# Performance work log

Hardware: AMD Instinct MI355X
Metric: run time of the kernel (lower is better)

The kernel has to match this reference:

```python
import jax, jax.numpy as jnp
import numpy as np

N = 100000
E = 800000
IN_DIM = 256
HEADS = 8
OUT_DIM = 32
OUT_ALL = HEADS * OUT_DIM  # 256 == IN_DIM -> residual is Identity
NEG_SLOPE = 0.2


def setup_inputs() -> dict:
    key = jax.random.key(0)
    ks = jax.random.split(key, 10)
    s_in = 1.0 / np.sqrt(IN_DIM)
    x = jax.random.normal(ks[0], (N, IN_DIM), dtype=jnp.float32)
    edge_index = jax.random.randint(ks[1], (2, E), 0, N, dtype=jnp.int64)
    Wl = jax.random.normal(ks[2], (IN_DIM, OUT_ALL), dtype=jnp.float32) * s_in
    bl = jnp.zeros((OUT_ALL,), dtype=jnp.float32)
    Wr = jax.random.normal(ks[3], (IN_DIM, OUT_ALL), dtype=jnp.float32) * s_in
    br = jnp.zeros((OUT_ALL,), dtype=jnp.float32)
    att = jax.random.normal(ks[4], (HEADS, OUT_DIM), dtype=jnp.float32) * (1.0 / np.sqrt(OUT_DIM))
    bias = jnp.zeros((OUT_ALL,), dtype=jnp.float32)
    gamma = jnp.ones((OUT_ALL,), dtype=jnp.float32)
    beta = jnp.zeros((OUT_ALL,), dtype=jnp.float32)
    return {"x": x, "edge_index": edge_index, "Wl": Wl, "bl": bl, "Wr": Wr,
            "br": br, "att": att, "bias": bias, "gamma": gamma, "beta": beta}


def reference(x, edge_index, Wl, bl, Wr, br, att, bias, gamma, beta):
    src, dst = edge_index[0], edge_index[1]
    # GATv2: separate transforms for source (lin_l) and target (lin_r)
    x_l = (x @ Wl + bl).reshape(N, HEADS, OUT_DIM)  # messages / source side
    x_r = (x @ Wr + br).reshape(N, HEADS, OUT_DIM)  # target side
    # edge-wise GATv2 score: a^T LeakyReLU(x_j + x_i)
    s = jax.nn.leaky_relu(x_l[src] + x_r[dst], NEG_SLOPE)  # [E, H, D]
    e = jnp.einsum('ehd,hd->eh', s, att)                   # [E, H]
    # segment softmax over incoming edges of each destination node
    m = jax.ops.segment_max(e, dst, num_segments=N)        # [N, H]
    p = jnp.exp(e - m[dst])                                # [E, H]
    denom = jax.ops.segment_sum(p, dst, num_segments=N)    # [N, H]
    denom = jnp.where(denom == 0, 1.0, denom)
    alpha = p / denom[dst]                                 # [E, H]
    # scatter-sum aggregate of alpha * lin_l(x_src)
    msg = alpha[:, :, None] * x_l[src]                     # [E, H, D]
    out = jax.ops.segment_sum(msg, dst, num_segments=N)    # [N, H, D]
    y = out.reshape(N, OUT_ALL) + bias
    # residual is Identity since in_dim == heads*out_dim
    z = y + x
    # LayerNorm then ELU
    mu = jnp.mean(z, axis=-1, keepdims=True)
    var = jnp.var(z, axis=-1, keepdims=True)
    zn = (z - mu) * jax.lax.rsqrt(var + 1e-5) * gamma + beta
    return jax.nn.elu(zn)
```

## Files before the change

### kernel.cpp

```cpp
#include <hip/hip_runtime.h>
#include <hip/hip_bf16.h>

#define NN 100000
#define EE 800000
#define DALL 256
#define NEG 0.2f

#define CNT_BLOCKS 3125
#define CVTW_BLOCKS 128
#define CVTX_BLOCKS 2048

typedef __attribute__((ext_vector_type(8))) short bf16x8;
typedef __attribute__((ext_vector_type(4))) float f32x4;

static __device__ __forceinline__ ushort f2b(float f) {
    __hip_bfloat16 h = __float2bfloat16(f);
    return *reinterpret_cast<ushort*>(&h);
}
static __device__ __forceinline__ float b2f(ushort u) {
    union { float f; unsigned v; } c; c.v = ((unsigned)u) << 16; return c.f;
}
static __device__ __forceinline__ void unpack8(uint4 u, float* v) {
    v[0] = b2f((ushort)(u.x & 0xffff)); v[1] = b2f((ushort)(u.x >> 16));
    v[2] = b2f((ushort)(u.y & 0xffff)); v[3] = b2f((ushort)(u.y >> 16));
    v[4] = b2f((ushort)(u.z & 0xffff)); v[5] = b2f((ushort)(u.z >> 16));
    v[6] = b2f((ushort)(u.w & 0xffff)); v[7] = b2f((ushort)(u.w >> 16));
}

__global__ __launch_bounds__(256) void fused_init(
    const float* __restrict__ x, const float* __restrict__ Wl,
    const float* __restrict__ Wr, const int* __restrict__ dst,
    ushort* __restrict__ xb, ushort* __restrict__ Wt, int* __restrict__ cnt)
{
    __shared__ float tile[32][33];
    int b = blockIdx.x;
    if (b < CNT_BLOCKS) {
        int e = b * 256 + threadIdx.x;
        if (e < EE) atomicAdd(&cnt[dst[e]], 1);
        return;
    }
    b -= CNT_BLOCKS;
    if (b < CVTW_BLOCKS) {
        int kt = (b & 7) * 32, nt = (b >> 3) * 32;
        int tx = threadIdx.x & 31, ty = threadIdx.x >> 5;
#pragma unroll
        for (int i = 0; i < 32; i += 8) {
            int k = kt + ty + i, n = nt + tx;
            float v = (n < 256) ? Wl[(size_t)k * 256 + n] : Wr[(size_t)k * 256 + (n - 256)];
            tile[ty + i][tx] = v;
        }
        __syncthreads();
#pragma unroll
        for (int i = 0; i < 32; i += 8) {
            int n = nt + ty + i, k = kt + tx;
            Wt[(size_t)n * 256 + k] = f2b(tile[tx][ty + i]);
        }
        return;
    }
    b -= CVTW_BLOCKS;
    const int total = NN * DALL / 8;
    for (int i = b * 256 + threadIdx.x; i < total; i += CVTX_BLOCKS * 256) {
        float4 a = reinterpret_cast<const float4*>(x)[i * 2];
        float4 c = reinterpret_cast<const float4*>(x)[i * 2 + 1];
        uint4 o;
        o.x = f2b(a.x) | ((unsigned)f2b(a.y) << 16);
        o.y = f2b(a.z) | ((unsigned)f2b(a.w) << 16);
        o.z = f2b(c.x) | ((unsigned)f2b(c.y) << 16);
        o.w = f2b(c.z) | ((unsigned)f2b(c.w) << 16);
        reinterpret_cast<uint4*>(xb)[i] = o;
    }
}

__global__ __launch_bounds__(256) void gemm_dual(
    const ushort* __restrict__ xb,
    const ushort* __restrict__ Wt,
    const float* __restrict__ bl, const float* __restrict__ br,
    ushort* __restrict__ xl, ushort* __restrict__ xr)
{
    __shared__ __align__(16) ushort smem[2][2][128 * 32];

    const int bx = blockIdx.x;
    const int rowBase = (bx >> 2) * 128;
    const int colBase = (bx & 3) * 128;
    const int t = threadIdx.x, lane = t & 63, wave = t >> 6;
    const int wr = (wave >> 1) * 64, wc = (wave & 1) * 64;

    const int sr  = lane >> 2;
    const int sc8 = (lane & 3) * 8;

    f32x4 acc[4][4];
#pragma unroll
    for (int m = 0; m < 4; ++m)
#pragma unroll
        for (int n = 0; n < 4; ++n) acc[m][n] = (f32x4){0.f, 0.f, 0.f, 0.f};

    auto STAGE = [&](int buf, int kb) {
#pragma unroll
        for (int tt = 0; tt < 2; ++tt) {
            int rbase = wave * 32 + tt * 16;
            int r = rbase + sr;
            int ga = rowBase + r; if (ga >= NN) ga = NN - 1;
            const ushort* gpA = xb + (size_t)ga * 256 + kb + sc8;
            ushort* lpA = &smem[buf][0][rbase * 32];
            __builtin_amdgcn_global_load_lds(
                (const __attribute__((address_space(1))) unsigned int*)gpA,
                (__attribute__((address_space(3))) unsigned int*)lpA, 16, 0, 0);
            int gb = colBase + r;
            const ushort* gpB = Wt + (size_t)gb * 256 + kb + sc8;
            ushort* lpB = &smem[buf][1][rbase * 32];
            __builtin_amdgcn_global_load_lds(
                (const __attribute__((address_space(1))) unsigned int*)gpB,
                (__attribute__((address_space(3))) unsigned int*)lpB, 16, 0, 0);
        }
    };

    STAGE(0, 0);
    __syncthreads();

#pragma unroll
    for (int s = 0; s < 8; ++s) {
        if (s < 7) STAGE((s + 1) & 1, (s + 1) * 32);
        const ushort* A = smem[s & 1][0];
        const ushort* B = smem[s & 1][1];
        bf16x8 af[4], bfr[4];
#pragma unroll
        for (int m = 0; m < 4; ++m)
            af[m] = *reinterpret_cast<const bf16x8*>(
                &A[(wr + m * 16 + (lane & 15)) * 32 + (lane >> 4) * 8]);
#pragma unroll
        for (int n = 0; n < 4; ++n)
            bfr[n] = *reinterpret_cast<const bf16x8*>(
                &B[(wc + n * 16 + (lane & 15)) * 32 + (lane >> 4) * 8]);
#pragma unroll
        for (int m = 0; m < 4; ++m)
#pragma unroll
            for (int n = 0; n < 4; ++n)
                acc[m][n] = __builtin_amdgcn_mfma_f32_16x16x32_bf16(
                    af[m], bfr[n], acc[m][n], 0, 0, 0);
        if (s < 7) __syncthreads();
    }

    const bool isL = (colBase < 256);
    ushort* OutP = isL ? xl : xr;
    const float* bvp = isL ? bl : br;
    const int cb0 = colBase & 255;

    int colLoc[4]; float bb[4];
#pragma unroll
    for (int n = 0; n < 4; ++n) {
        colLoc[n] = cb0 + wc + n * 16 + (lane & 15);
        bb[n] = bvp[colLoc[n]];
    }
#pragma unroll
    for (int m = 0; m < 4; ++m) {
        int r0 = rowBase + wr + m * 16 + (lane >> 4) * 4;
#pragma unroll
        for (int r = 0; r < 4; ++r) {
            int row = r0 + r;
            if (row < NN) {
#pragma unroll
                for (int n = 0; n < 4; ++n)
                    OutP[(size_t)row * 256 + colLoc[n]] = f2b(acc[m][n][r] + bb[n]);
            }
        }
    }
}

__global__ __launch_bounds__(256) void scan_part1(const int* __restrict__ cnt,
                                                  int* __restrict__ bsums)
{
    __shared__ int red[256];
    int base = blockIdx.x * 1024 + threadIdx.x * 4;
    int s = 0;
#pragma unroll
    for (int k = 0; k < 4; ++k) { int i = base + k; if (i < NN) s += cnt[i]; }
    red[threadIdx.x] = s; __syncthreads();
    for (int off = 128; off > 0; off >>= 1) {
        if (threadIdx.x < off) red[threadIdx.x] += red[threadIdx.x + off];
        __syncthreads();
    }
    if (threadIdx.x == 0) bsums[blockIdx.x] = red[0];
}

__global__ __launch_bounds__(256) void scan_rowptr(const int* __restrict__ cnt,
                                                   const int* __restrict__ bsums,
                                                   int* __restrict__ rowptr)
{
    __shared__ int redB[256];
    __shared__ int pre[256];
    int tb = threadIdx.x;
    redB[tb] = (tb < (int)blockIdx.x) ? bsums[tb] : 0;
    __syncthreads();
    for (int off = 128; off > 0; off >>= 1) {
        if (tb < off) redB[tb] += redB[tb + off];
        __syncthreads();
    }
    int base0 = redB[0];

    int base = blockIdx.x * 1024 + tb * 4;
    int v[4]; int s = 0;
#pragma unroll
    for (int k = 0; k < 4; ++k) { int i = base + k; v[k] = (i < NN) ? cnt[i] : 0; s += v[k]; }
    pre[tb] = s; __syncthreads();
    for (int off = 1; off < 256; off <<= 1) {
        int tv = (tb >= off) ? pre[tb - off] : 0;
        __syncthreads();
        pre[tb] += tv;
        __syncthreads();
    }
    int excl = pre[tb] - s + base0;
#pragma unroll
    for (int k = 0; k < 4; ++k) {
        int i = base + k;
        if (i < NN) { rowptr[i] = excl; excl += v[k]; }
    }
}

__global__ __launch_bounds__(256) void fill_csr(const int* __restrict__ src,
                                                const int* __restrict__ dst,
                                                int* __restrict__ rowptr,
                                                int* __restrict__ srcs)
{
    int e = blockIdx.x * 256 + threadIdx.x;
    if (e >= EE) return;
    int pos = atomicAdd(&rowptr[dst[e]], 1);
    srcs[pos] = src[e];
}

__global__ __launch_bounds__(256) void aggregate_finalize(
    const ushort* __restrict__ xl, const ushort* __restrict__ xr,
    const int* __restrict__ srcs, const int* __restrict__ rowptr,
    const float* __restrict__ att, const ushort* __restrict__ xb,
    const float* __restrict__ bias, const float* __restrict__ gamma,
    const float* __restrict__ beta, float* __restrict__ out)
{
    int node = blockIdx.x * 4 + (threadIdx.x >> 6);
    if (node >= NN) return;
    int lane = threadIdx.x & 63;
    int half = lane >> 5;
    int dl = lane & 31;
    const int off = dl * 8;

    uint4 xru = *reinterpret_cast<const uint4*>(xr + (size_t)node * DALL + off);
    float xrv[8]; unpack8(xru, xrv);
    float atv[8];
    {
        float4 a0 = *reinterpret_cast<const float4*>(att + off);
        float4 a1 = *reinterpret_cast<const float4*>(att + off + 4);
        atv[0]=a0.x; atv[1]=a0.y; atv[2]=a0.z; atv[3]=a0.w;
        atv[4]=a1.x; atv[5]=a1.y; atv[6]=a1.z; atv[7]=a1.w;
    }

    int beg = node ? rowptr[node - 1] : 0;
    int end = rowptr[node];
    float a[8] = {0.f,0.f,0.f,0.f,0.f,0.f,0.f,0.f};
    float dsum = 0.f;

    for (int base = beg; base < end; base += 8) {
        int j0 = base + half;
        int j1 = base + 2 + half;
        int j2 = base + 4 + half;
        int j3 = base + 6 + half;
        bool k0 = j0 < end, k1 = j1 < end, k2 = j2 < end, k3 = j3 < end;
        int s0 = srcs[k0 ? j0 : beg];
        int s1 = srcs[k1 ? j1 : beg];
        int s2 = srcs[k2 ? j2 : beg];
        int s3 = srcs[k3 ? j3 : beg];
        uint4 g0 = *reinterpret_cast<const uint4*>(xl + (size_t)s0 * DALL + off);
        uint4 g1 = *reinterpret_cast<const uint4*>(xl + (size_t)s1 * DALL + off);
        uint4 g2 = *reinterpret_cast<const uint4*>(xl + (size_t)s2 * DALL + off);
        uint4 g3 = *reinterpret_cast<const uint4*>(xl + (size_t)s3 * DALL + off);
        float v0v[8], v1v[8], v2v[8], v3v[8];
        unpack8(g0, v0v); unpack8(g1, v1v); unpack8(g2, v2v); unpack8(g3, v3v);
        float p0 = 0.f, p1 = 0.f, p2 = 0.f, p3 = 0.f;
#pragma unroll
        for (int i = 0; i < 8; ++i) {
            float z0 = v0v[i] + xrv[i]; p0 += fmaxf(z0, NEG * z0) * atv[i];
            float z1 = v1v[i] + xrv[i]; p1 += fmaxf(z1, NEG * z1) * atv[i];
            float z2 = v2v[i] + xrv[i]; p2 += fmaxf(z2, NEG * z2) * atv[i];
            float z3 = v3v[i] + xrv[i]; p3 += fmaxf(z3, NEG * z3) * atv[i];
        }
        p0 += __shfl_xor(p0, 1); p0 += __shfl_xor(p0, 2);
        p1 += __shfl_xor(p1, 1); p1 += __shfl_xor(p1, 2);
        p2 += __shfl_xor(p2, 1); p2 += __shfl_xor(p2, 2);
        p3 += __shfl_xor(p3, 1); p3 += __shfl_xor(p3, 2);
        float e0 = k0 ? __expf(p0) : 0.f;
        float e1 = k1 ? __expf(p1) : 0.f;
        float e2 = k2 ? __expf(p2) : 0.f;
        float e3 = k3 ? __expf(p3) : 0.f;
#pragma unroll
        for (int i = 0; i < 8; ++i)
            a[i] += e0 * v0v[i] + e1 * v1v[i] + e2 * v2v[i] + e3 * v3v[i];
        dsum += e0 + e1 + e2 + e3;
    }

#pragma unroll
    for (int i = 0; i < 8; ++i) a[i] += __shfl_xor(a[i], 32);
    dsum += __shfl_xor(dsum, 32);
    float inv = dsum > 0.f ? 1.f / dsum : 0.f;

    uint4 xbu = *reinterpret_cast<const uint4*>(xb + (size_t)node * DALL + off);
    float xv[8]; unpack8(xbu, xv);
    float bvv[8], gvv[8], bev[8];
    {
        float4 b0 = *reinterpret_cast<const float4*>(bias + off);
        float4 b1 = *reinterpret_cast<const float4*>(bias + off + 4);
        bvv[0]=b0.x; bvv[1]=b0.y; bvv[2]=b0.z; bvv[3]=b0.w;
        bvv[4]=b1.x; bvv[5]=b1.y; bvv[6]=b1.z; bvv[7]=b1.w;
        float4 g0 = *reinterpret_cast<const float4*>(gamma + off);
        float4 g1 = *reinterpret_cast<const float4*>(gamma + off + 4);
        gvv[0]=g0.x; gvv[1]=g0.y; gvv[2]=g0.z; gvv[3]=g0.w;
        gvv[4]=g1.x; gvv[5]=g1.y; gvv[6]=g1.z; gvv[7]=g1.w;
        float4 e0 = *reinterpret_cast<const float4*>(beta + off);
        float4 e1 = *reinterpret_cast<const float4*>(beta + off + 4);
        bev[0]=e0.x; bev[1]=e0.y; bev[2]=e0.z; bev[3]=e0.w;
        bev[4]=e1.x; bev[5]=e1.y; bev[6]=e1.z; bev[7]=e1.w;
    }

    float y[8]; float sum = 0.f, sq = 0.f;
#pragma unroll
    for (int i = 0; i < 8; ++i) {
        y[i] = a[i] * inv + bvv[i] + xv[i];
        sum += y[i]; sq += y[i] * y[i];
    }
#pragma unroll
    for (int m = 1; m < 32; m <<= 1) {
        sum += __shfl_xor(sum, m);
        sq  += __shfl_xor(sq, m);
    }
    float mu  = sum * (1.0f / 256.0f);
    float var = sq * (1.0f / 256.0f) - mu * mu;
    float rr  = rsqrtf(var + 1e-5f);

    if (half == 0) {
        float4 o0, o1;
        float z0 = (y[0]-mu)*rr*gvv[0] + bev[0];
        float z1 = (y[1]-mu)*rr*gvv[1] + bev[1];
        float z2 = (y[2]-mu)*rr*gvv[2] + bev[2];
        float z3 = (y[3]-mu)*rr*gvv[3] + bev[3];
        float z4 = (y[4]-mu)*rr*gvv[4] + bev[4];
        float z5 = (y[5]-mu)*rr*gvv[5] + bev[5];
        float z6 = (y[6]-mu)*rr*gvv[6] + bev[6];
        float z7 = (y[7]-mu)*rr*gvv[7] + bev[7];
        o0.x = z0 > 0.f ? z0 : expm1f(z0);
        o0.y = z1 > 0.f ? z1 : expm1f(z1);
        o0.z = z2 > 0.f ? z2 : expm1f(z2);
        o0.w = z3 > 0.f ? z3 : expm1f(z3);
        o1.x = z4 > 0.f ? z4 : expm1f(z4);
        o1.y = z5 > 0.f ? z5 : expm1f(z5);
        o1.z = z6 > 0.f ? z6 : expm1f(z6);
        o1.w = z7 > 0.f ? z7 : expm1f(z7);
        *reinterpret_cast<float4*>(out + (size_t)node * DALL + off)     = o0;
        *reinterpret_cast<float4*>(out + (size_t)node * DALL + off + 4) = o1;
    }
}

extern "C" void kernel_launch(void* const* d_in, const int* in_sizes, int n_in,
                              void* d_out, int out_size, void* d_ws, size_t ws_size,
                              hipStream_t stream)
{
    const float* x    = (const float*)d_in[0];
    const int*   edge = (const int*)d_in[1];
    const float* Wl   = (const float*)d_in[2];
    const float* bl   = (const float*)d_in[3];
    const float* Wr   = (const float*)d_in[4];
    const float* br   = (const float*)d_in[5];
    const float* att  = (const float*)d_in[6];
    const float* bias = (const float*)d_in[7];
    const float* gamma= (const float*)d_in[8];
    const float* beta = (const float*)d_in[9];
    float* out = (float*)d_out;

    const int* srcIdx = edge;
    const int* dstIdx = edge + EE;

    ushort* xl = (ushort*)d_ws;
    ushort* xr = xl + (size_t)NN * DALL;
    ushort* xb = xr + (size_t)NN * DALL;
    ushort* Wt = xb + (size_t)NN * DALL;
    int* rowptr = (int*)(Wt + 512 * 256);
    int* cnt    = rowptr + NN + 1;
    int* srcs   = cnt + NN;
    int* bsums  = srcs + EE;

    const int SCAN_NB = (NN + 1023) / 1024;

    hipMemsetAsync(cnt, 0, NN * sizeof(int), stream);
    fused_init<<<CNT_BLOCKS + CVTW_BLOCKS + CVTX_BLOCKS, 256, 0, stream>>>(
        x, Wl, Wr, dstIdx, xb, Wt, cnt);
    gemm_dual<<<782 * 4, 256, 0, stream>>>(xb, Wt, bl, br, xl, xr);
    scan_part1<<<SCAN_NB, 256, 0, stream>>>(cnt, bsums);
    scan_rowptr<<<SCAN_NB, 256, 0, stream>>>(cnt, bsums, rowptr);
    fill_csr<<<(EE + 255) / 256, 256, 0, stream>>>(srcIdx, dstIdx, rowptr, srcs);
    aggregate_finalize<<<NN / 4, 256, 0, stream>>>(
        xl, xr, srcs, rowptr, att, xb, bias, gamma, beta, out);
}
```

Before: 306.3 us.

## Widen GEMM tile to 128x256 with 512 threads and halve aggregate unroll

The dual GEMM now uses 512-thread blocks that each compute a 128x256 output tile, so one block covers a full lin_l or lin_r half and the A tile of x is staged once per half instead of twice, with staging redistributed across 8 waves. The edge aggregation loop processes 4 edges per iteration (2 per half-wave) instead of 8, which lowers register pressure and wasted masked loads on low-degree nodes at the cost of less memory-level parallelism. The larger block needs more LDS per block and may reduce how many blocks fit per CU.

```diff
diff --git a/kernel.cpp b/kernel.cpp
--- a/kernel.cpp
+++ b/kernel.cpp
@@ -71,22 +71,21 @@
     }
 }
 
-__global__ __launch_bounds__(256) void gemm_dual(
+__global__ __launch_bounds__(512) void gemm_dual(
     const ushort* __restrict__ xb,
     const ushort* __restrict__ Wt,
     const float* __restrict__ bl, const float* __restrict__ br,
     ushort* __restrict__ xl, ushort* __restrict__ xr)
 {
-    __shared__ __align__(16) ushort smem[2][2][128 * 32];
+    __shared__ __align__(16) ushort smemA[2][128 * 32];
+    __shared__ __align__(16) ushort smemB[2][256 * 32];
 
     const int bx = blockIdx.x;
-    const int rowBase = (bx >> 2) * 128;
-    const int colBase = (bx & 3) * 128;
+    const int rowBase = (bx >> 1) * 128;
+    const int colBase = (bx & 1) * 256;
     const int t = threadIdx.x, lane = t & 63, wave = t >> 6;
-    const int wr = (wave >> 1) * 64, wc = (wave & 1) * 64;
-
-    const int sr  = lane >> 2;
-    const int sc8 = (lane & 3) * 8;
+    const int wr = (wave >> 2) * 64;
+    const int wc = (wave & 3) * 64;
 
     f32x4 acc[4][4];
 #pragma unroll
@@ -95,22 +94,24 @@
         for (int n = 0; n < 4; ++n) acc[m][n] = (f32x4){0.f, 0.f, 0.f, 0.f};
 
     auto STAGE = [&](int buf, int kb) {
-#pragma unroll
-        for (int tt = 0; tt < 2; ++tt) {
-            int rbase = wave * 32 + tt * 16;
-            int r = rbase + sr;
-            int ga = rowBase + r; if (ga >= NN) ga = NN - 1;
-            const ushort* gpA = xb + (size_t)ga * 256 + kb + sc8;
-            ushort* lpA = &smem[buf][0][rbase * 32];
+        {
+            int rc = t >> 2, slot = t & 3;
+            int ga = rowBase + rc; if (ga >= NN) ga = NN - 1;
+            const ushort* gp = xb + (size_t)ga * 256 + kb + slot * 8;
+            ushort* lp = &smemA[buf][wave * 512];
             __builtin_amdgcn_global_load_lds(
-                (const __attribute__((address_space(1))) unsigned int*)gpA,
-                (__attribute__((address_space(3))) unsigned int*)lpA, 16, 0, 0);
-            int gb = colBase + r;
-            const ushort* gpB = Wt + (size_t)gb * 256 + kb + sc8;
-            ushort* lpB = &smem[buf][1][rbase * 32];
+                (const __attribute__((address_space(1))) unsigned int*)gp,
+                (__attribute__((address_space(3))) unsigned int*)lp, 16, 0, 0);
+        }
+#pragma unroll
+        for (int i = 0; i < 2; ++i) {
+            int c = i * 512 + t;
+            int rc = c >> 2, slot = c & 3;
+            const ushort* gp = Wt + (size_t)(colBase + rc) * 256 + kb + slot * 8;
+            ushort* lp = &smemB[buf][(i * 512 + wave * 64) * 8];
             __builtin_amdgcn_global_load_lds(
-                (const __attribute__((address_space(1))) unsigned int*)gpB,
-                (__attribute__((address_space(3))) unsigned int*)lpB, 16, 0, 0);
+                (const __attribute__((address_space(1))) unsigned int*)gp,
+                (__attribute__((address_space(3))) unsigned int*)lp, 16, 0, 0);
         }
     };
 
@@ -120,8 +121,8 @@
 #pragma unroll
     for (int s = 0; s < 8; ++s) {
         if (s < 7) STAGE((s + 1) & 1, (s + 1) * 32);
-        const ushort* A = smem[s & 1][0];
-        const ushort* B = smem[s & 1][1];
+        const ushort* A = smemA[s & 1];
+        const ushort* B = smemB[s & 1];
         bf16x8 af[4], bfr[4];
 #pragma unroll
         for (int m = 0; m < 4; ++m)
@@ -140,15 +141,14 @@
         if (s < 7) __syncthreads();
     }
 
-    const bool isL = (colBase < 256);
+    const bool isL = (colBase == 0);
     ushort* OutP = isL ? xl : xr;
     const float* bvp = isL ? bl : br;
-    const int cb0 = colBase & 255;
 
     int colLoc[4]; float bb[4];
 #pragma unroll
     for (int n = 0; n < 4; ++n) {
-        colLoc[n] = cb0 + wc + n * 16 + (lane & 15);
+        colLoc[n] = wc + n * 16 + (lane & 15);
         bb[n] = bvp[colLoc[n]];
     }
 #pragma unroll
@@ -256,42 +256,28 @@
     float a[8] = {0.f,0.f,0.f,0.f,0.f,0.f,0.f,0.f};
     float dsum = 0.f;
 
-    for (int base = beg; base < end; base += 8) {
-        int j0 = base + half;
-        int j1 = base + 2 + half;
-        int j2 = base + 4 + half;
-        int j3 = base + 6 + half;
-        bool k0 = j0 < end, k1 = j1 < end, k2 = j2 < end, k3 = j3 < end;
-        int s0 = srcs[k0 ? j0 : beg];
-        int s1 = srcs[k1 ? j1 : beg];
-        int s2 = srcs[k2 ? j2 : beg];
-        int s3 = srcs[k3 ? j3 : beg];
-        uint4 g0 = *reinterpret_cast<const uint4*>(xl + (size_t)s0 * DALL + off);
-        uint4 g1 = *reinterpret_cast<const uint4*>(xl + (size_t)s1 * DALL + off);
-        uint4 g2 = *reinterpret_cast<const uint4*>(xl + (size_t)s2 * DALL + off);
-        uint4 g3 = *reinterpret_cast<const uint4*>(xl + (size_t)s3 * DALL + off);
-        float v0v[8], v1v[8], v2v[8], v3v[8];
-        unpack8(g0, v0v); unpack8(g1, v1v); unpack8(g2, v2v); unpack8(g3, v3v);
-        float p0 = 0.f, p1 = 0.f, p2 = 0.f, p3 = 0.f;
+    for (int base = beg; base < end; base += 4) {
+        int jA = base + half;
+        int jB = base + 2 + half;
+        bool vA = jA < end, vB = jB < end;
+        int sA = srcs[vA ? jA : beg];
+        int sB = srcs[vB ? jB : beg];
+        uint4 gA = *reinterpret_cast<const uint4*>(xl + (size_t)sA * DALL + off);
+        uint4 gB = *reinterpret_cast<const uint4*>(xl + (size_t)sB * DALL + off);
+        float vAv[8], vBv[8]; unpack8(gA, vAv); unpack8(gB, vBv);
+        float pA = 0.f, pB = 0.f;
 #pragma unroll
         for (int i = 0; i < 8; ++i) {
-            float z0 = v0v[i] + xrv[i]; p0 += fmaxf(z0, NEG * z0) * atv[i];
-            float z1 = v1v[i] + xrv[i]; p1 += fmaxf(z1, NEG * z1) * atv[i];
-            float z2 = v2v[i] + xrv[i]; p2 += fmaxf(z2, NEG * z2) * atv[i];
-            float z3 = v3v[i] + xrv[i]; p3 += fmaxf(z3, NEG * z3) * atv[i];
-        }
-        p0 += __shfl_xor(p0, 1); p0 += __shfl_xor(p0, 2);
-        p1 += __shfl_xor(p1, 1); p1 += __shfl_xor(p1, 2);
-        p2 += __shfl_xor(p2, 1); p2 += __shfl_xor(p2, 2);
-        p3 += __shfl_xor(p3, 1); p3 += __shfl_xor(p3, 2);
-        float e0 = k0 ? __expf(p0) : 0.f;
-        float e1 = k1 ? __expf(p1) : 0.f;
-        float e2 = k2 ? __expf(p2) : 0.f;
-        float e3 = k3 ? __expf(p3) : 0.f;
-#pragma unroll
-        for (int i = 0; i < 8; ++i)
-            a[i] += e0 * v0v[i] + e1 * v1v[i] + e2 * v2v[i] + e3 * v3v[i];
-        dsum += e0 + e1 + e2 + e3;
+            float z = vAv[i] + xrv[i];  pA += fmaxf(z, NEG * z) * atv[i];
+            float z2 = vBv[i] + xrv[i]; pB += fmaxf(z2, NEG * z2) * atv[i];
+        }
+        pA += __shfl_xor(pA, 1); pA += __shfl_xor(pA, 2);
+        pB += __shfl_xor(pB, 1); pB += __shfl_xor(pB, 2);
+        float peA = vA ? __expf(pA) : 0.f;
+        float peB = vB ? __expf(pB) : 0.f;
+#pragma unroll
+        for (int i = 0; i < 8; ++i) a[i] += peA * vAv[i] + peB * vBv[i];
+        dsum += peA + peB;
     }
 
 #pragma unroll
@@ -388,7 +374,7 @@
     hipMemsetAsync(cnt, 0, NN * sizeof(int), stream);
     fused_init<<<CNT_BLOCKS + CVTW_BLOCKS + CVTX_BLOCKS, 256, 0, stream>>>(
         x, Wl, Wr, dstIdx, xb, Wt, cnt);
-    gemm_dual<<<782 * 4, 256, 0, stream>>>(xb, Wt, bl, br, xl, xr);
+    gemm_dual<<<782 * 2, 512, 0, stream>>>(xb, Wt, bl, br, xl, xr);
     scan_part1<<<SCAN_NB, 256, 0, stream>>>(cnt, bsums);
     scan_rowptr<<<SCAN_NB, 256, 0, stream>>>(cnt, bsums, rowptr);
     fill_csr<<<(EE + 255) / 256, 256, 0, stream>>>(srcIdx, dstIdx, rowptr, srcs);
```

Result: faster. 280.3 us (-8.5%).
